# Optimization experiments

Measured on AMD Instinct MI355X. Metric: run time of the kernel, lower is better.

The kernel has to match this reference:

```python
import jax, jax.numpy as jnp
import numpy as np

N, E, D = 50000, 600000, 128

def _lin(key, fan_in, fan_out):
    kw, kb = jax.random.split(key)
    s = 1.0 / np.sqrt(fan_in)
    W = jax.random.uniform(kw, (fan_in, fan_out), minval=-s, maxval=s, dtype=jnp.float32)
    b = jax.random.uniform(kb, (fan_out,), minval=-s, maxval=s, dtype=jnp.float32)
    return W, b

def setup_inputs() -> dict:
    key = jax.random.key(0)
    ks = jax.random.split(key, 16)
    h = jax.random.normal(ks[0], (N, D), dtype=jnp.float32)
    pos = jax.random.normal(ks[1], (N, 2), dtype=jnp.float32)
    edge_index = jax.random.randint(ks[2], (2, E), 0, N, dtype=jnp.int64)
    edge_attr = jax.random.uniform(ks[3], (E, 1), dtype=jnp.float32)
    Wq, bq = _lin(ks[4], D, D)
    Wk, bk = _lin(ks[5], D, D)
    Wv, bv = _lin(ks[6], D, D)
    We1, be1 = _lin(ks[7], 1, D)
    We2, be2 = _lin(ks[8], D, D)
    Wa1, ba1 = _lin(ks[9], 3 * D, D)
    Wa2, ba2 = _lin(ks[10], D, 1)
    Wm1, bm1 = _lin(ks[11], 2 * D, D)
    Wm2, bm2 = _lin(ks[12], D, D)
    return dict(h=h, pos=pos, edge_index=edge_index, edge_attr=edge_attr,
                Wq=Wq, bq=bq, Wk=Wk, bk=bk, Wv=Wv, bv=bv,
                We1=We1, be1=be1, We2=We2, be2=be2,
                Wa1=Wa1, ba1=ba1, Wa2=Wa2, ba2=ba2,
                Wm1=Wm1, bm1=bm1, Wm2=Wm2, bm2=bm2)

def reference(h, pos, edge_index, edge_attr,
              Wq, bq, Wk, bk, Wv, bv,
              We1, be1, We2, be2,
              Wa1, ba1, Wa2, ba2,
              Wm1, bm1, Wm2, bm2):
    row, col = edge_index[0], edge_index[1]  # source, destination
    q = h @ Wq + bq                          # [N, D]
    k = h @ Wk + bk
    v = h @ Wv + bv
    e = jax.nn.relu(edge_attr @ We1 + be1) @ We2 + be2  # [E, D]
    # per-edge attention logits
    attn_in = jnp.concatenate([q[col], k[row], e], axis=-1)          # [E, 3D]
    logits = (jax.nn.relu(attn_in @ Wa1 + ba1) @ Wa2 + ba2)[:, 0]    # [E]
    # segment softmax grouped by destination node (torch_geometric style)
    seg_max = jax.ops.segment_max(logits, col, num_segments=N)       # [N]
    ex = jnp.exp(logits - seg_max[col])
    seg_sum = jax.ops.segment_sum(ex, col, num_segments=N)           # [N]
    w = ex / (seg_sum[col] + 1e-16)                                  # [E]
    # per-edge messages
    msg_in = jnp.concatenate([v[row], e], axis=-1)                   # [E, 2D]
    msg = jax.nn.silu(msg_in @ Wm1 + bm1) @ Wm2 + bm2                # [E, D]
    agg = jax.ops.segment_sum(msg * w[:, None], col, num_segments=N) # [N, D]
    return (h + agg, pos)
```

## Files before the change

### kernel.cpp

```cpp
#include <hip/hip_runtime.h>
#include <math.h>

#define D 128
#define SB 256

typedef __attribute__((ext_vector_type(8))) short bf16x8;
typedef __attribute__((ext_vector_type(4))) float f32x4;

__device__ inline unsigned f2bf(float f) {
    unsigned u = __float_as_uint(f);
    return (u + 0x7FFFu + ((u >> 16) & 1u)) >> 16;
}

__global__ __launch_bounds__(256) void prep(
    const float* __restrict__ Wq, const float* __restrict__ bq,
    const float* __restrict__ Wk, const float* __restrict__ bk,
    const float* __restrict__ Wv, const float* __restrict__ bv,
    const float* __restrict__ Wa1, const float* __restrict__ ba1,
    const float* __restrict__ Wm1, const float* __restrict__ bm1,
    const float* __restrict__ We1, const float* __restrict__ be1,
    const float* __restrict__ We2, const float* __restrict__ be2,
    const float* __restrict__ Wm2,
    const int* __restrict__ ei, int E,
    ushort* __restrict__ Wpk, ushort* __restrict__ Wpk2,
    float* __restrict__ bqa, float* __restrict__ bka, float* __restrict__ bva,
    float* __restrict__ bounds,
    float2* __restrict__ AB, float2* __restrict__ MB,
    int* __restrict__ deg)
{
    __shared__ float smem[1536];
    int b = blockIdx.x;
    int t = threadIdx.x;
    int j = t & 127, half = t >> 7;
    if (b < 384) {
        int which = b >> 7, i = b & 127;
        const float *A, *B;
        if (which == 0)      { A = Wq; B = Wa1; }
        else if (which == 1) { A = Wk; B = Wa1 + 128 * D; }
        else                 { A = Wv; B = Wm1; }
        float acc = 0.f;
        for (int k = half * 64; k < half * 64 + 64; k++) acc += A[i * D + k] * B[k * D + j];
        smem[t] = acc;
        __syncthreads();
        if (half == 0) {
            float v = smem[j] + smem[128 + j];
            int gc = which * 128 + j;
            int nt = gc >> 4;
            int ks = i >> 5;
            int lane = (((i >> 3) & 3) << 4) | (gc & 15);
            int j8 = i & 7;
            Wpk[((nt * 4 + ks) * 64 + lane) * 8 + j8] = (ushort)f2bf(v);
        }
    } else if (b < 387) {
        int which = b - 384;
        const float *bias, *B, *extra; float *out;
        if (which == 0)      { bias = bq; B = Wa1;           out = bqa; extra = ba1; }
        else if (which == 1) { bias = bk; B = Wa1 + 128 * D; out = bka; extra = nullptr; }
        else                 { bias = bv; B = Wm1;           out = bva; extra = bm1; }
        float acc = 0.f;
        for (int k = half * 64; k < half * 64 + 64; k++) acc += bias[k] * B[k * D + j];
        smem[t] = acc;
        __syncthreads();
        if (half == 0) out[j] = smem[j] + smem[128 + j] + (extra ? extra[j] : 0.f);
    } else if (b == 387) {
        float* sb = smem;
        if (t < 128) {
            float w = We1[t], bb = be1[t];
            float th = (w != 0.f) ? (-bb / w) : 2.f;
            sb[t] = fminf(fmaxf(th, 0.f), 1.f);
        }
        __syncthreads();
        for (int k = 2; k <= 128; k <<= 1)
            for (int jj = k >> 1; jj > 0; jj >>= 1) {
                if (t < 128) {
                    int ixj = t ^ jj;
                    if (ixj > t) {
                        float a = sb[t], c = sb[ixj];
                        bool up = ((t & k) == 0);
                        if (up ? (a > c) : (a < c)) { sb[t] = c; sb[ixj] = a; }
                    }
                }
                __syncthreads();
            }
        if (t == 0) { bounds[0] = 0.f; bounds[129] = 1.f; }
        if (t < 128) bounds[1 + t] = sb[t];
    } else if (b < 517) {
        float* sb = smem;
        float* Ae = smem + 128;
        float* Be = smem + 256;
        float* P  = smem + 384;
        if (t < 128) {
            float w = We1[t], bb = be1[t];
            float th = (w != 0.f) ? (-bb / w) : 2.f;
            sb[t] = fminf(fmaxf(th, 0.f), 1.f);
        }
        __syncthreads();
        for (int k = 2; k <= 128; k <<= 1)
            for (int jj = k >> 1; jj > 0; jj >>= 1) {
                if (t < 128) {
                    int ixj = t ^ jj;
                    if (ixj > t) {
                        float a = sb[t], c = sb[ixj];
                        bool up = ((t & k) == 0);
                        if (up ? (a > c) : (a < c)) { sb[t] = c; sb[ixj] = a; }
                    }
                }
                __syncthreads();
            }
        int i = b - 388;
        float lo = (i == 0)   ? 0.f : sb[i - 1];
        float hi = (i == 128) ? 1.f : sb[i];
        float m = 0.5f * (lo + hi);
        float ae = 0.f, be = 0.f;
        for (int k = half * 64; k < half * 64 + 64; k++) {
            float ww = We1[k], bb2 = be1[k];
            if (m * ww + bb2 > 0.f) { ae += ww * We2[k * D + j]; be += bb2 * We2[k * D + j]; }
        }
        P[t] = ae; P[256 + t] = be;
        __syncthreads();
        if (half == 0) {
            Ae[j] = P[j] + P[128 + j];
            Be[j] = P[256 + j] + P[384 + j] + be2[j];
        }
        __syncthreads();
        float aa = 0.f, ba = 0.f, am = 0.f, bm = 0.f;
        for (int l2 = half * 64; l2 < half * 64 + 64; l2++) {
            float ael = Ae[l2], bel = Be[l2];
            float wa = Wa1[(256 + l2) * D + j];
            float wm = Wm1[(128 + l2) * D + j];
            aa += ael * wa; ba += bel * wa;
            am += ael * wm; bm += bel * wm;
        }
        P[t] = aa; P[256 + t] = ba; P[512 + t] = am; P[768 + t] = bm;
        __syncthreads();
        if (half == 0) {
            AB[i * 128 + j] = make_float2(P[j] + P[128 + j], P[256 + j] + P[384 + j]);
            MB[i * 128 + j] = make_float2(P[512 + j] + P[640 + j], P[768 + j] + P[896 + j]);
        }
    } else if (b < 645) {
        if (t < 128) {
            int i = b - 517;
            int nt = t >> 4;
            int ks = i >> 5;
            int lane = (((i >> 3) & 3) << 4) | (t & 15);
            int j8 = i & 7;
            Wpk2[((nt * 4 + ks) * 64 + lane) * 8 + j8] = (ushort)f2bf(Wm2[i * D + t]);
        }
    } else {
        int e = (b - 645) * 256 + t;
        if (e < E) atomicAdd(deg + ei[E + e], 1);
    }
}

__global__ __launch_bounds__(SB) void k_scan1(const int* __restrict__ deg, int N,
                                              int* __restrict__ partial)
{
    __shared__ int ls[SB];
    int t = threadIdx.x;
    int i = blockIdx.x * SB + t;
    ls[t] = (i < N) ? deg[i] : 0;
    __syncthreads();
    for (int s = SB / 2; s > 0; s >>= 1) {
        if (t < s) ls[t] += ls[t + s];
        __syncthreads();
    }
    if (t == 0) partial[blockIdx.x] = ls[0];
}

__global__ __launch_bounds__(SB) void k_scan23(const int* __restrict__ deg, int N,
                                               const int* __restrict__ partial, int NB,
                                               int* __restrict__ off)
{
    __shared__ int lp[SB];
    __shared__ int ls[SB];
    int t = threadIdx.x;
    int pv = (t < NB) ? partial[t] : 0;
    lp[t] = pv;
    __syncthreads();
    int pval = pv;
    for (int s = 1; s < SB; s <<= 1) {
        int add = (t >= s) ? lp[t - s] : 0;
        __syncthreads();
        pval += add;
        lp[t] = pval;
        __syncthreads();
    }
    int base = (blockIdx.x > 0) ? lp[blockIdx.x - 1] : 0;

    int i = blockIdx.x * SB + t;
    int v = (i < N) ? deg[i] : 0;
    ls[t] = v;
    __syncthreads();
    int val = v;
    for (int s = 1; s < SB; s <<= 1) {
        int add = (t >= s) ? ls[t - s] : 0;
        __syncthreads();
        val += add;
        ls[t] = val;
        __syncthreads();
    }
    if (i < N) off[i] = base + val - v;
}

__global__ __launch_bounds__(256) void k_scatter(const int* __restrict__ ei,
                                                 const float* __restrict__ eattr, int E,
                                                 const float* __restrict__ bounds,
                                                 int* __restrict__ off, int2* __restrict__ recs)
{
    __shared__ float bnd[130];
    int t = threadIdx.x;
    if (t < 130) bnd[t] = bounds[t];
    __syncthreads();
    int e = blockIdx.x * 256 + t;
    if (e >= E) return;
    int row = ei[e], col = ei[E + e];
    float a = eattr[e];
    int lo = 0, hi = 128;
    while (lo < hi) { int mid = (lo + hi + 1) >> 1; if (bnd[mid] <= a) lo = mid; else hi = mid - 1; }
    int p = atomicAdd(off + col, 1);
    recs[p] = make_int2(row | (lo << 17), __float_as_int(a));
}

__global__ __launch_bounds__(256) void node_gemm(
    const float* __restrict__ h, int N,
    const ushort* __restrict__ Wpk,
    const float* __restrict__ bqa, const float* __restrict__ bka, const float* __restrict__ bva,
    ushort* __restrict__ qb, unsigned* __restrict__ kv)
{
    __shared__ __align__(16) ushort hsb[64 * 128];
    int t = threadIdx.x;
    int row0 = blockIdx.x * 64;
#pragma unroll
    for (int i = 0; i < 4; i++) {
        int g = t + i * 256;
        int r = g >> 4, c = g & 15;
        int grow = row0 + r;
        float4 f0, f1;
        if (grow < N) {
            const float4* hp = (const float4*)(h + (size_t)grow * D + c * 8);
            f0 = hp[0]; f1 = hp[1];
        } else {
            f0 = make_float4(0.f, 0.f, 0.f, 0.f); f1 = f0;
        }
        ushort u[8] = { (ushort)f2bf(f0.x), (ushort)f2bf(f0.y), (ushort)f2bf(f0.z), (ushort)f2bf(f0.w),
                        (ushort)f2bf(f1.x), (ushort)f2bf(f1.y), (ushort)f2bf(f1.z), (ushort)f2bf(f1.w) };
        int pc = c ^ (r & 15);
        *(uint4*)&hsb[r * 128 + pc * 8] = *(uint4*)u;
    }
    __syncthreads();

    int w = t >> 6, l = t & 63;
    int lrow = w * 16 + (l & 15);
    f32x4 acc[24];
#pragma unroll
    for (int i = 0; i < 24; i++) acc[i] = (f32x4){0.f, 0.f, 0.f, 0.f};

    const bf16x8* WB = (const bf16x8*)Wpk;
#pragma unroll
    for (int ks = 0; ks < 4; ks++) {
        int c = (ks * 4 + (l >> 4)) ^ (l & 15);
        bf16x8 afrag = *(const bf16x8*)&hsb[lrow * 128 + c * 8];
#pragma unroll
        for (int nt = 0; nt < 24; nt++) {
            bf16x8 bfrag = WB[(nt * 4 + ks) * 64 + l];
            acc[nt] = __builtin_amdgcn_mfma_f32_16x16x32_bf16(afrag, bfrag, acc[nt], 0, 0, 0);
        }
    }

    int rbase = row0 + w * 16 + ((l >> 4) << 2);
    int cl = l & 15;
#pragma unroll
    for (int cc = 0; cc < 8; cc++) {
        float bqv = bqa[cc * 16 + cl];
        float bkv = bka[cc * 16 + cl];
        float bvv = bva[cc * 16 + cl];
        f32x4 aq = acc[cc], ak = acc[8 + cc], av = acc[16 + cc];
#pragma unroll
        for (int r = 0; r < 4; r++) {
            int row = rbase + r;
            if (row < N) {
                qb[(size_t)row * D + cc * 16 + cl] = (ushort)f2bf(aq[r] + bqv);
                kv[(size_t)row * D + cc * 16 + cl] =
                    (f2bf(av[r] + bvv) << 16) | f2bf(ak[r] + bkv);
            }
        }
    }
}

__global__ __launch_bounds__(256) void node_all(
    const int2* __restrict__ recs, int N,
    const int* __restrict__ off,
    const ushort* __restrict__ qb, const unsigned* __restrict__ kv,
    const float2* __restrict__ AB, const float2* __restrict__ MB,
    const float* __restrict__ Wa2,
    unsigned* __restrict__ Sb, float* __restrict__ segsum)
{
    int t = threadIdx.x;
    int lane = t & 63;
    int slot = lane >> 5;
    int l = lane & 31;
    int n = blockIdx.x * 4 + (t >> 6);
    if (n >= N) return;
    int end = off[n];
    int start = (n > 0) ? off[n - 1] : 0;

    const char* kvc = (const char*)kv;
    const char* ABc = (const char*)AB;
    const char* MBc = (const char*)MB;

    uint2 qp = *(const uint2*)(qb + (size_t)n * D + 4 * l);
    float q0 = __uint_as_float(qp.x << 16);
    float q1 = __uint_as_float(qp.x & 0xFFFF0000u);
    float q2 = __uint_as_float(qp.y << 16);
    float q3 = __uint_as_float(qp.y & 0xFFFF0000u);
    float4 w4 = *(const float4*)(Wa2 + 4 * l);

    float m_run = -INFINITY;
    float a0 = 0.f, a1 = 0.f, a2 = 0.f, a3 = 0.f, ssum = 0.f;

    for (int idx = start; idx < end; idx += 4) {
        int i1 = idx + slot;
        int i2 = idx + 2 + slot;
        bool lv1 = i1 < end, lv2 = i2 < end;
        int2 rec1 = recs[lv1 ? i1 : start];
        int2 rec2 = recs[lv2 ? i2 : start];
        unsigned u1 = (unsigned)rec1.x, u2 = (unsigned)rec2.x;
        float at1 = __int_as_float(rec1.y), at2 = __int_as_float(rec2.y);
        int rb1 = (int)(u1 & 0x1FFFFu) << 9, tb1 = (int)(u1 >> 17) << 10;
        int rb2 = (int)(u2 & 0x1FFFFu) << 9, tb2 = (int)(u2 >> 17) << 10;

        uint4 kp1 = *(const uint4*)(kvc + rb1 + (l << 4));
        uint4 kp2 = *(const uint4*)(kvc + rb2 + (l << 4));
        float4 ab0a = *(const float4*)(ABc + tb1 + (l << 5));
        float4 ab1a = *(const float4*)(ABc + tb1 + (l << 5) + 16);
        float4 mb0a = *(const float4*)(MBc + tb1 + (l << 5));
        float4 mb1a = *(const float4*)(MBc + tb1 + (l << 5) + 16);
        float4 ab0b = *(const float4*)(ABc + tb2 + (l << 5));
        float4 ab1b = *(const float4*)(ABc + tb2 + (l << 5) + 16);
        float4 mb0b = *(const float4*)(MBc + tb2 + (l << 5));
        float4 mb1b = *(const float4*)(MBc + tb2 + (l << 5) + 16);

        float p1 = fmaxf(q0 + __uint_as_float(kp1.x << 16) + at1 * ab0a.x + ab0a.y, 0.f) * w4.x
                 + fmaxf(q1 + __uint_as_float(kp1.y << 16) + at1 * ab0a.z + ab0a.w, 0.f) * w4.y
                 + fmaxf(q2 + __uint_as_float(kp1.z << 16) + at1 * ab1a.x + ab1a.y, 0.f) * w4.z
                 + fmaxf(q3 + __uint_as_float(kp1.w << 16) + at1 * ab1a.z + ab1a.w, 0.f) * w4.w;
        float p2 = fmaxf(q0 + __uint_as_float(kp2.x << 16) + at2 * ab0b.x + ab0b.y, 0.f) * w4.x
                 + fmaxf(q1 + __uint_as_float(kp2.y << 16) + at2 * ab0b.z + ab0b.w, 0.f) * w4.y
                 + fmaxf(q2 + __uint_as_float(kp2.z << 16) + at2 * ab1b.x + ab1b.y, 0.f) * w4.z
                 + fmaxf(q3 + __uint_as_float(kp2.w << 16) + at2 * ab1b.z + ab1b.w, 0.f) * w4.w;
#pragma unroll
        for (int s = 1; s < 32; s <<= 1) {
            p1 += __shfl_xor(p1, s, 64);
            p2 += __shfl_xor(p2, s, 64);
        }
        float pm1 = lv1 ? p1 : -INFINITY;
        float pm2 = lv2 ? p2 : -INFINITY;
        float pmx = fmaxf(pm1, pm2);
        pmx = fmaxf(pmx, __shfl_xor(pmx, 32, 64));
        if (pmx - m_run > 8.f) {
            float mN = fmaxf(m_run, pmx);
            float sc = __expf(m_run - mN);
            a0 *= sc; a1 *= sc; a2 *= sc; a3 *= sc; ssum *= sc;
            m_run = mN;
        }
        float ex1 = __expf(pm1 - m_run);
        float ex2 = __expf(pm2 - m_run);

        float x0 = __uint_as_float(kp1.x & 0xFFFF0000u) + at1 * mb0a.x + mb0a.y;
        float x1 = __uint_as_float(kp1.y & 0xFFFF0000u) + at1 * mb0a.z + mb0a.w;
        float x2 = __uint_as_float(kp1.z & 0xFFFF0000u) + at1 * mb1a.x + mb1a.y;
        float x3 = __uint_as_float(kp1.w & 0xFFFF0000u) + at1 * mb1a.z + mb1a.w;
        float y0 = __uint_as_float(kp2.x & 0xFFFF0000u) + at2 * mb0b.x + mb0b.y;
        float y1 = __uint_as_float(kp2.y & 0xFFFF0000u) + at2 * mb0b.z + mb0b.w;
        float y2 = __uint_as_float(kp2.z & 0xFFFF0000u) + at2 * mb1b.x + mb1b.y;
        float y3 = __uint_as_float(kp2.w & 0xFFFF0000u) + at2 * mb1b.z + mb1b.w;
        float s10 = x0 * __builtin_amdgcn_rcpf(1.f + __expf(-x0));
        float s11 = x1 * __builtin_amdgcn_rcpf(1.f + __expf(-x1));
        float s12 = x2 * __builtin_amdgcn_rcpf(1.f + __expf(-x2));
        float s13 = x3 * __builtin_amdgcn_rcpf(1.f + __expf(-x3));
        float s20 = y0 * __builtin_amdgcn_rcpf(1.f + __expf(-y0));
        float s21 = y1 * __builtin_amdgcn_rcpf(1.f + __expf(-y1));
        float s22 = y2 * __builtin_amdgcn_rcpf(1.f + __expf(-y2));
        float s23 = y3 * __builtin_amdgcn_rcpf(1.f + __expf(-y3));

        a0 = fmaf(ex2, s20, fmaf(ex1, s10, a0));
        a1 = fmaf(ex2, s21, fmaf(ex1, s11, a1));
        a2 = fmaf(ex2, s22, fmaf(ex1, s12, a2));
        a3 = fmaf(ex2, s23, fmaf(ex1, s13, a3));
        ssum += ex1 + ex2;
    }

    a0 += __shfl_xor(a0, 32, 64);
    a1 += __shfl_xor(a1, 32, 64);
    a2 += __shfl_xor(a2, 32, 64);
    a3 += __shfl_xor(a3, 32, 64);
    ssum += __shfl_xor(ssum, 32, 64);

    if (slot == 0) {
        float inv = __builtin_amdgcn_rcpf(ssum + 1e-16f);
        unsigned pw0 = f2bf(a0 * inv) | (f2bf(a1 * inv) << 16);
        unsigned pw1 = f2bf(a2 * inv) | (f2bf(a3 * inv) << 16);
        *(uint2*)(Sb + (size_t)n * 64 + 2 * l) = make_uint2(pw0, pw1);
        if (l == 0) segsum[n] = ssum;
    }
}

__global__ __launch_bounds__(256) void node_out(
    const float* __restrict__ h, int N,
    const unsigned* __restrict__ Sb, const ushort* __restrict__ Wpk2,
    const float* __restrict__ bm2, const float* __restrict__ segsum,
    float* __restrict__ out, const float* __restrict__ pos, int npos, int G1)
{
    int b = blockIdx.x;
    int t = threadIdx.x;
    if (b >= G1) {
        int i = ((b - G1) * 256 + t) * 4;
        float* outp = out + (size_t)N * D;
        if (i + 3 < npos) {
            *(float4*)(outp + i) = *(const float4*)(pos + i);
        } else {
            for (int j = i; j < npos; j++) outp[j] = pos[j];
        }
        return;
    }
    __shared__ __align__(16) ushort ssb[64 * 128];
    int row0 = b * 64;
#pragma unroll
    for (int i = 0; i < 4; i++) {
        int g = t + i * 256;
        int r = g >> 4, c = g & 15;
        int grow = row0 + r;
        uint4 u = make_uint4(0u, 0u, 0u, 0u);
        if (grow < N) u = *(const uint4*)(Sb + (size_t)grow * 64 + c * 4);
        int pc = c ^ (r & 15);
        *(uint4*)&ssb[r * 128 + pc * 8] = u;
    }
    __syncthreads();

    int w = t >> 6, l = t & 63;
    int lrow = w * 16 + (l & 15);
    f32x4 acc[8];
#pragma unroll
    for (int i = 0; i < 8; i++) acc[i] = (f32x4){0.f, 0.f, 0.f, 0.f};

    const bf16x8* WB = (const bf16x8*)Wpk2;
#pragma unroll
    for (int ks = 0; ks < 4; ks++) {
        int c = (ks * 4 + (l >> 4)) ^ (l & 15);
        bf16x8 afrag = *(const bf16x8*)&ssb[lrow * 128 + c * 8];
#pragma unroll
        for (int nt = 0; nt < 8; nt++) {
            bf16x8 bfrag = WB[(nt * 4 + ks) * 64 + l];
            acc[nt] = __builtin_amdgcn_mfma_f32_16x16x32_bf16(afrag, bfrag, acc[nt], 0, 0, 0);
        }
    }

    int rbase = row0 + w * 16 + ((l >> 4) << 2);
    int cl = l & 15;
#pragma unroll
    for (int cc = 0; cc < 8; cc++) {
        float bb = bm2[cc * 16 + cl];
        f32x4 av = acc[cc];
#pragma unroll
        for (int r = 0; r < 4; r++) {
            int row = rbase + r;
            if (row < N) {
                float ws_ = segsum[row];
                ws_ = ws_ / (ws_ + 1e-16f);
                out[(size_t)row * D + cc * 16 + cl] =
                    h[(size_t)row * D + cc * 16 + cl] + av[r] + bb * ws_;
            }
        }
    }
}

extern "C" void kernel_launch(void* const* d_in, const int* in_sizes, int n_in,
                              void* d_out, int out_size, void* d_ws, size_t ws_size,
                              hipStream_t stream)
{
    const float* h     = (const float*)d_in[0];
    const float* pos   = (const float*)d_in[1];
    const int*   ei    = (const int*)d_in[2];
    const float* eattr = (const float*)d_in[3];
    const float* Wq  = (const float*)d_in[4];  const float* bq  = (const float*)d_in[5];
    const float* Wk  = (const float*)d_in[6];  const float* bk  = (const float*)d_in[7];
    const float* Wv  = (const float*)d_in[8];  const float* bv  = (const float*)d_in[9];
    const float* We1 = (const float*)d_in[10]; const float* be1 = (const float*)d_in[11];
    const float* We2 = (const float*)d_in[12]; const float* be2 = (const float*)d_in[13];
    const float* Wa1 = (const float*)d_in[14]; const float* ba1 = (const float*)d_in[15];
    const float* Wa2 = (const float*)d_in[16];
    const float* Wm1 = (const float*)d_in[18]; const float* bm1 = (const float*)d_in[19];
    const float* Wm2 = (const float*)d_in[20]; const float* bm2 = (const float*)d_in[21];

    int N = in_sizes[0] / D;
    int E = in_sizes[3];
    int NB = (N + SB - 1) / SB;

    float* ws = (float*)d_ws;
    size_t off_f = 0;
    auto alloc = [&](size_t n) { float* p = ws + off_f; off_f += (n + 63) & ~(size_t)63; return p; };

    ushort* Wpk  = (ushort*)alloc(24 * 4 * 64 * 8 / 2);
    ushort* Wpk2 = (ushort*)alloc(8 * 4 * 64 * 8 / 2);
    float* bqa = alloc(D); float* bka = alloc(D); float* bva = alloc(D);
    float* bounds = alloc(130);
    float2* AB = (float2*)alloc((size_t)129 * 128 * 2);
    float2* MB = (float2*)alloc((size_t)129 * 128 * 2);
    ushort* qb = (ushort*)alloc((size_t)N * 64);
    unsigned* kv = (unsigned*)alloc((size_t)N * D);
    unsigned* Sb = (unsigned*)alloc((size_t)N * 64);
    float* segsum = alloc(N);
    int* deg  = (int*)alloc(N);
    int* offs = (int*)alloc(N);
    int* partial = (int*)alloc(256);
    int2* recs = (int2*)alloc((size_t)E * 2);

    hipMemsetAsync(deg, 0, (size_t)N * 4, stream);

    int HB = (E + 255) / 256;
    prep<<<645 + HB, 256, 0, stream>>>(Wq, bq, Wk, bk, Wv, bv, Wa1, ba1, Wm1, bm1,
                                       We1, be1, We2, be2, Wm2, ei, E,
                                       Wpk, Wpk2, bqa, bka, bva, bounds, AB, MB, deg);

    k_scan1<<<NB, SB, 0, stream>>>(deg, N, partial);
    k_scan23<<<NB, SB, 0, stream>>>(deg, N, partial, NB, offs);

    node_gemm<<<(N + 63) / 64, 256, 0, stream>>>(h, N, Wpk, bqa, bka, bva, qb, kv);

    k_scatter<<<(E + 255) / 256, 256, 0, stream>>>(ei, eattr, E, bounds, offs, recs);

    node_all<<<(N + 3) / 4, 256, 0, stream>>>(recs, N, offs, qb, kv, AB, MB, Wa2,
                                              Sb, segsum);

    int G1 = (N + 63) / 64;
    int G2 = (2 * N + 1023) / 1024;
    node_out<<<G1 + G2, 256, 0, stream>>>(h, N, Sb, Wpk2, bm2, segsum, (float*)d_out,
                                          pos, 2 * N, G1);
}
```

Before: 259.9 us.

## Map one destination node per half-wave in node_all instead of per wavefront

Result: faster. 245.2 us, median of 2 (-5.7%).

```diff
diff --git a/kernel.cpp b/kernel.cpp
--- a/kernel.cpp
+++ b/kernel.cpp
@@ -296,19 +296,20 @@
     unsigned* __restrict__ Sb, float* __restrict__ segsum)
 {
     int t = threadIdx.x;
-    int lane = t & 63;
-    int slot = lane >> 5;
-    int l = lane & 31;
-    int n = blockIdx.x * 4 + (t >> 6);
-    if (n >= N) return;
-    int end = off[n];
-    int start = (n > 0) ? off[n - 1] : 0;
+    int l = t & 31;
+    int n = blockIdx.x * 8 + (t >> 5);
+    bool valid = (n < N);
+    int start = 0, end = 0;
+    if (valid) {
+        end = off[n];
+        start = (n > 0) ? off[n - 1] : 0;
+    }
 
     const char* kvc = (const char*)kv;
     const char* ABc = (const char*)AB;
     const char* MBc = (const char*)MB;
 
-    uint2 qp = *(const uint2*)(qb + (size_t)n * D + 4 * l);
+    uint2 qp = valid ? *(const uint2*)(qb + (size_t)n * D + 4 * l) : make_uint2(0u, 0u);
     float q0 = __uint_as_float(qp.x << 16);
     float q1 = __uint_as_float(qp.x & 0xFFFF0000u);
     float q2 = __uint_as_float(qp.y << 16);
@@ -318,12 +319,10 @@
     float m_run = -INFINITY;
     float a0 = 0.f, a1 = 0.f, a2 = 0.f, a3 = 0.f, ssum = 0.f;
 
-    for (int idx = start; idx < end; idx += 4) {
-        int i1 = idx + slot;
-        int i2 = idx + 2 + slot;
-        bool lv1 = i1 < end, lv2 = i2 < end;
-        int2 rec1 = recs[lv1 ? i1 : start];
-        int2 rec2 = recs[lv2 ? i2 : start];
+    int idx = start;
+    for (; idx + 2 <= end; idx += 2) {
+        int2 rec1 = recs[idx];
+        int2 rec2 = recs[idx + 1];
         unsigned u1 = (unsigned)rec1.x, u2 = (unsigned)rec2.x;
         float at1 = __int_as_float(rec1.y), at2 = __int_as_float(rec2.y);
         int rb1 = (int)(u1 & 0x1FFFFu) << 9, tb1 = (int)(u1 >> 17) << 10;
@@ -353,18 +352,14 @@
             p1 += __shfl_xor(p1, s, 64);
             p2 += __shfl_xor(p2, s, 64);
         }
-        float pm1 = lv1 ? p1 : -INFINITY;
-        float pm2 = lv2 ? p2 : -INFINITY;
-        float pmx = fmaxf(pm1, pm2);
-        pmx = fmaxf(pmx, __shfl_xor(pmx, 32, 64));
-        if (pmx - m_run > 8.f) {
-            float mN = fmaxf(m_run, pmx);
+        float d1 = p1 - m_run, d2 = p2 - m_run;
+        if (fmaxf(d1, d2) > 8.f) {
+            float mN = fmaxf(fmaxf(p1, p2), m_run);
             float sc = __expf(m_run - mN);
             a0 *= sc; a1 *= sc; a2 *= sc; a3 *= sc; ssum *= sc;
-            m_run = mN;
-        }
-        float ex1 = __expf(pm1 - m_run);
-        float ex2 = __expf(pm2 - m_run);
+            m_run = mN; d1 = p1 - mN; d2 = p2 - mN;
+        }
+        float ex1 = __expf(d1), ex2 = __expf(d2);
 
         float x0 = __uint_as_float(kp1.x & 0xFFFF0000u) + at1 * mb0a.x + mb0a.y;
         float x1 = __uint_as_float(kp1.y & 0xFFFF0000u) + at1 * mb0a.z + mb0a.w;
@@ -389,14 +384,42 @@
         a3 = fmaf(ex2, s23, fmaf(ex1, s13, a3));
         ssum += ex1 + ex2;
     }
-
-    a0 += __shfl_xor(a0, 32, 64);
-    a1 += __shfl_xor(a1, 32, 64);
-    a2 += __shfl_xor(a2, 32, 64);
-    a3 += __shfl_xor(a3, 32, 64);
-    ssum += __shfl_xor(ssum, 32, 64);
-
-    if (slot == 0) {
+    if (idx < end) {
+        int2 rec = recs[idx];
+        unsigned u1 = (unsigned)rec.x;
+        float a = __int_as_float(rec.y);
+        int rb = (int)(u1 & 0x1FFFFu) << 9, tb = (int)(u1 >> 17) << 10;
+        uint4 kp = *(const uint4*)(kvc + rb + (l << 4));
+        float4 ab0 = *(const float4*)(ABc + tb + (l << 5));
+        float4 ab1 = *(const float4*)(ABc + tb + (l << 5) + 16);
+        float4 mb0 = *(const float4*)(MBc + tb + (l << 5));
+        float4 mb1 = *(const float4*)(MBc + tb + (l << 5) + 16);
+        float p1 = fmaxf(q0 + __uint_as_float(kp.x << 16) + a * ab0.x + ab0.y, 0.f) * w4.x
+                 + fmaxf(q1 + __uint_as_float(kp.y << 16) + a * ab0.z + ab0.w, 0.f) * w4.y
+                 + fmaxf(q2 + __uint_as_float(kp.z << 16) + a * ab1.x + ab1.y, 0.f) * w4.z
+                 + fmaxf(q3 + __uint_as_float(kp.w << 16) + a * ab1.z + ab1.w, 0.f) * w4.w;
+#pragma unroll
+        for (int s = 1; s < 32; s <<= 1) p1 += __shfl_xor(p1, s, 64);
+        float d1 = p1 - m_run;
+        if (d1 > 8.f) {
+            float mN = p1;
+            float sc = __expf(m_run - mN);
+            a0 *= sc; a1 *= sc; a2 *= sc; a3 *= sc; ssum *= sc;
+            m_run = mN; d1 = 0.f;
+        }
+        float ex = __expf(d1);
+        float x0 = __uint_as_float(kp.x & 0xFFFF0000u) + a * mb0.x + mb0.y;
+        float x1 = __uint_as_float(kp.y & 0xFFFF0000u) + a * mb0.z + mb0.w;
+        float x2 = __uint_as_float(kp.z & 0xFFFF0000u) + a * mb1.x + mb1.y;
+        float x3 = __uint_as_float(kp.w & 0xFFFF0000u) + a * mb1.z + mb1.w;
+        a0 = fmaf(ex, x0 * __builtin_amdgcn_rcpf(1.f + __expf(-x0)), a0);
+        a1 = fmaf(ex, x1 * __builtin_amdgcn_rcpf(1.f + __expf(-x1)), a1);
+        a2 = fmaf(ex, x2 * __builtin_amdgcn_rcpf(1.f + __expf(-x2)), a2);
+        a3 = fmaf(ex, x3 * __builtin_amdgcn_rcpf(1.f + __expf(-x3)), a3);
+        ssum += ex;
+    }
+
+    if (valid) {
         float inv = __builtin_amdgcn_rcpf(ssum + 1e-16f);
         unsigned pw0 = f2bf(a0 * inv) | (f2bf(a1 * inv) << 16);
         unsigned pw1 = f2bf(a2 * inv) | (f2bf(a3 * inv) << 16);
@@ -529,7 +552,7 @@
 
     k_scatter<<<(E + 255) / 256, 256, 0, stream>>>(ei, eattr, E, bounds, offs, recs);
 
-    node_all<<<(N + 3) / 4, 256, 0, stream>>>(recs, N, offs, qb, kv, AB, MB, Wa2,
+    node_all<<<(N + 7) / 8, 256, 0, stream>>>(recs, N, offs, qb, kv, AB, MB, Wa2,
                                               Sb, segsum);
 
     int G1 = (N + 63) / 64;
```
